# Kernel optimization log

Hardware: AMD Instinct MI355X
Metric: run time of the kernel (lower is better)

Reference implementation:

```python
import jax, jax.numpy as jnp
import numpy as np

B, L, C = 4, 2048, 1024
H = 16
D = C // H  # head_dim = 64


def _rope(t, cos, sin):
    # t: [B, H, L, D]; cos/sin: [L, D//2] broadcast to [1, 1, L, D//2]
    te = t[..., ::2]
    to = t[..., 1::2]
    c = cos[None, None]
    s = sin[None, None]
    re = te * c - to * s
    ro = te * s + to * c
    # interleave even/odd back: [..., D//2, 2] -> [..., D]
    return jnp.stack([re, ro], axis=-1).reshape(t.shape)


def setup_inputs() -> dict:
    key = jax.random.key(0)
    ks = jax.random.split(key, 5)
    x = jax.random.normal(ks[0], (B, L, C), dtype=jnp.float32)
    # rotary phases: theta_i = 10000^(-2i/D), angles = pos * theta
    inv_freq = 1.0 / (10000.0 ** (np.arange(0, D, 2, dtype=np.float32) / D))
    ang = np.arange(L, dtype=np.float32)[:, None] * inv_freq[None, :]  # [L, D//2]
    cos = jnp.asarray(np.cos(ang))
    sin = jnp.asarray(np.sin(ang))
    w_qkv = jax.random.normal(ks[1], (3 * C, C), dtype=jnp.float32) * (C ** -0.5)
    w_proj = jax.random.normal(ks[2], (C, C), dtype=jnp.float32) * (C ** -0.5)
    b_proj = jnp.zeros((C,), dtype=jnp.float32)
    return {"x": x, "cos": cos, "sin": sin, "w_qkv": w_qkv, "w_proj": w_proj, "b_proj": b_proj}


def reference(x, cos, sin, w_qkv, w_proj, b_proj):
    Bx, Lx, Cx = x.shape
    # QKV projection (torch Linear: y = x @ W.T), then split heads
    qkv = jnp.einsum("blc,fc->blf", x, w_qkv)  # [B, L, 3C]
    qkv = qkv.reshape(Bx, Lx, 3, H, D).transpose(2, 0, 3, 1, 4)  # [3, B, H, L, D]
    q, k, v = qkv[0], qkv[1], qkv[2]
    q = _rope(q, cos, sin)
    k = _rope(k, cos, sin)
    # scaled dot-product attention, non-causal
    scale = D ** -0.5
    scores = jnp.einsum("bhqd,bhkd->bhqk", q, k) * scale
    attn = jax.nn.softmax(scores, axis=-1)
    o = jnp.einsum("bhqk,bhkd->bhqd", attn, v)  # [B, H, L, D]
    o = o.transpose(0, 2, 1, 3).reshape(Bx, Lx, Cx)
    return jnp.einsum("blc,fc->blf", o, w_proj) + b_proj
```

## Files before the change

kernel.cpp:

```cpp
#include <hip/hip_runtime.h>
#include <hip/hip_bf16.h>
#include <cstdint>


typedef unsigned short u16;
typedef __attribute__((ext_vector_type(8))) short bf16x8;
typedef __attribute__((ext_vector_type(4))) float f32x4;
typedef __attribute__((ext_vector_type(2))) unsigned int u32x2;

#define GLD16(g, l)                                                            \
  __builtin_amdgcn_global_load_lds(                                            \
      (const __attribute__((address_space(1))) void*)(g),                      \
      (__attribute__((address_space(3))) void*)(l), 16, 0, 0)

static __device__ __forceinline__ u16 f32_bf16(float f) {
  union { float f; unsigned u; } v; v.f = f;
  unsigned r = v.u + 0x7FFFu + ((v.u >> 16) & 1u);
  return (u16)(r >> 16);
}
static __device__ __forceinline__ float bf16_f32(u16 h) {
  union { unsigned u; float f; } v; v.u = ((unsigned)h) << 16;
  return v.f;
}
static __device__ __forceinline__ unsigned pack_rne(float a, float b) {
  union { float f; unsigned u; } x, y; x.f = a; y.f = b;
  unsigned ua = x.u + 0x7FFFu + ((x.u >> 16) & 1u);
  unsigned ub = y.u + 0x7FFFu + ((y.u >> 16) & 1u);
  return (ua >> 16) | (ub & 0xFFFF0000u);
}
static __device__ __forceinline__ unsigned pack_bf16_hw(float a, float b) {
  float2 t; t.x = a; t.y = b;
  __hip_bfloat162 h = __float22bfloat162_rn(t);
  union { __hip_bfloat162 h; unsigned u; } c; c.h = h;
  return c.u;
}

__global__ __launch_bounds__(256) void convert_all(
    const void* __restrict__ x, const void* __restrict__ wq,
    const void* __restrict__ wp, const void* __restrict__ cs,
    const void* __restrict__ sn, const void* __restrict__ bs,
    u16* __restrict__ xb, u16* __restrict__ wqb, u16* __restrict__ wpb,
    u16* __restrict__ cb, u16* __restrict__ sb, u16* __restrict__ bb) {
  const unsigned f32mode = (((const unsigned*)cs)[0] == 0x3F800000u);
  int blk = blockIdx.x;
  if (blk >= 12288 && blk < 12416) {
    const void* src = (blk < 12352) ? cs : sn;
    u16* dst = (blk < 12352) ? cb : sb;
    int i = (blk - ((blk < 12352) ? 12288 : 12352)) * 256 + threadIdx.x;
    u16 e[4];
    if (f32mode) {
      float4 v = ((const float4*)src)[i];
      const float* vf = (const float*)&v;
#pragma unroll
      for (int c = 0; c < 4; c++) e[c] = f32_bf16(vf[c]);
    } else {
      uint2 v = ((const uint2*)src)[i];
      e[0] = (u16)(v.x & 0xFFFFu); e[1] = (u16)(v.x >> 16);
      e[2] = (u16)(v.y & 0xFFFFu); e[3] = (u16)(v.y >> 16);
    }
#pragma unroll
    for (int c = 0; c < 4; c++) {
      int E = i * 4 + c;
      dst[(E & 31) * 2048 + (E >> 5)] = e[c];
    }
    return;
  }
  const void* src; u16* dst; int i0, n4;
  if (blk < 8192)       { src = x;  dst = xb;  i0 = blk;         n4 = 2097152; }
  else if (blk < 11264) { src = wq; dst = wqb; i0 = blk - 8192;  n4 = 786432; }
  else if (blk < 12288) { src = wp; dst = wpb; i0 = blk - 11264; n4 = 262144; }
  else                  { src = bs; dst = bb;  i0 = blk - 12416; n4 = 256; }
  int i = i0 * 256 + threadIdx.x;
  if (i >= n4) return;
  if (f32mode) {
    float4 v = ((const float4*)src)[i];
    uint2 o;
    o.x = pack_rne(v.x, v.y);
    o.y = pack_rne(v.z, v.w);
    ((uint2*)dst)[i] = o;
  } else {
    ((uint2*)dst)[i] = ((const uint2*)src)[i];
  }
}

static __device__ __forceinline__ void gemm_mainloop(
    const u16* __restrict__ A, const u16* __restrict__ Bm, int K,
    int m0, int n0, u16* As, u16* Bs, f32x4 acc[4][4]) {
  const int tid  = threadIdx.x;
  const int lane = tid & 63;
  const int wave = tid >> 6;
  const int n16  = lane & 15;
  const int quad = lane >> 4;
  const int wm = (wave >> 1) * 64;
  const int wn = (wave & 1) * 64;
  const u16* ag = A  + (size_t)(m0 + wave * 16 + (lane >> 2)) * K + (lane & 3) * 8;
  const u16* bg = Bm + (size_t)(n0 + wave * 16 + (lane >> 2)) * K + (lane & 3) * 8;
  u16* al = As + wave * (16 * 32);
  u16* bl = Bs + wave * (16 * 32);
  for (int kt = 0; kt < K; kt += 32) {
    GLD16(ag + kt, al);
    GLD16(ag + (size_t)64 * K + kt, al + 64 * 32);
    GLD16(bg + kt, bl);
    GLD16(bg + (size_t)64 * K + kt, bl + 64 * 32);
    __syncthreads();
    bf16x8 af[4], bf[4];
#pragma unroll
    for (int i = 0; i < 4; i++)
      af[i] = *(const bf16x8*)(As + (wm + i * 16 + n16) * 32 + quad * 8);
#pragma unroll
    for (int j = 0; j < 4; j++)
      bf[j] = *(const bf16x8*)(Bs + (wn + j * 16 + n16) * 32 + quad * 8);
#pragma unroll
    for (int i = 0; i < 4; i++)
#pragma unroll
      for (int j = 0; j < 4; j++)
        acc[i][j] = __builtin_amdgcn_mfma_f32_16x16x32_bf16(af[i], bf[j], acc[i][j], 0, 0, 0);
    __syncthreads();
  }
}

__global__ __launch_bounds__(256) void gemm_qkv(
    const u16* __restrict__ x, const u16* __restrict__ w,
    u16* __restrict__ q_ws, u16* __restrict__ k_ws, u16* __restrict__ vt_ws,
    const u16* __restrict__ cosT, const u16* __restrict__ sinT) {
  __shared__ u16 As[128 * 32];
  __shared__ u16 Bs[128 * 32];
  f32x4 acc[4][4];
#pragma unroll
  for (int i = 0; i < 4; i++)
#pragma unroll
    for (int j = 0; j < 4; j++) acc[i][j] = (f32x4){0.f, 0.f, 0.f, 0.f};
  const int m0 = blockIdx.y * 128;
  const int n0 = blockIdx.x * 128;
  gemm_mainloop(x, w, 1024, m0, n0, As, Bs, acc);
  const int lane = threadIdx.x & 63, wave = threadIdx.x >> 6;
  const int n16 = lane & 15, quad = lane >> 4;
  const int wm = (wave >> 1) * 64, wn = (wave & 1) * 64;
#pragma unroll
  for (int i = 0; i < 4; i++)
#pragma unroll
    for (int j = 0; j < 4; j++) {
      int f = n0 + wn + j * 16 + n16;
      int which = f >> 10;
      int rem = f & 1023;
      int h = rem >> 6, d = rem & 63;
      int l0 = m0 + wm + i * 16 + quad * 4;
      int b = l0 >> 11, l = l0 & 2047;
      if (which == 2) {
        uint2 o;
        o.x = pack_rne(acc[i][j][0], acc[i][j][1]);
        o.y = pack_rne(acc[i][j][2], acc[i][j][3]);
        size_t idx = (((size_t)b * 16 + h) * 64 + d) * 2048 + l;
        *(uint2*)(vt_ws + idx) = o;
      } else {
        u16* dst = (which == 0) ? q_ws : k_ws;
        const float sc = (which == 0) ? 0.18033688011112042f : 1.0f;
        const int ip = d >> 1;
        const bool ev = !(d & 1);
        uint2 cu = *(const uint2*)(cosT + ip * 2048 + l);
        uint2 su = *(const uint2*)(sinT + ip * 2048 + l);
        float cf[4] = {bf16_f32((u16)(cu.x & 0xFFFFu)), bf16_f32((u16)(cu.x >> 16)),
                       bf16_f32((u16)(cu.y & 0xFFFFu)), bf16_f32((u16)(cu.y >> 16))};
        float sf[4] = {bf16_f32((u16)(su.x & 0xFFFFu)), bf16_f32((u16)(su.x >> 16)),
                       bf16_f32((u16)(su.y & 0xFFFFu)), bf16_f32((u16)(su.y >> 16))};
        size_t base = (((size_t)b * 16 + h) * 2048 + l) * 64 + d;
#pragma unroll
        for (int r = 0; r < 4; r++) {
          float v = acc[i][j][r];
          float p = __shfl_xor(v, 1, 64);
          float o = ev ? (v * cf[r] - p * sf[r]) : (p * sf[r] + v * cf[r]);
          dst[base + (size_t)r * 64] = f32_bf16(o * sc);
        }
      }
    }
}

__global__ __launch_bounds__(256, 4) void flash_attn(
    const u16* __restrict__ q_ws, const u16* __restrict__ k_ws,
    const u16* __restrict__ vt_ws, u16* __restrict__ o_ws) {
  __shared__ u16 Ks[2][64 * 64];
  __shared__ u16 Vs[2][64 * 64];
  const int bh = blockIdx.x & 63;
  const int q0 = (blockIdx.x >> 6) * 128;
  const int b = bh >> 4, h = bh & 15;
  const int tid = threadIdx.x, lane = tid & 63, wave = tid >> 6;
  const int n16 = lane & 15, quad = lane >> 4;
  const int x7 = n16 & 7;
  const int pn16 = (n16 & 3) | ((n16 & 4) << 1) | ((n16 & 8) >> 1);
  const int px7 = pn16 & 7;
  const size_t hoff = (size_t)bh * (2048 * 64);

  bf16x8 qf[2][2];
#pragma unroll
  for (int qb = 0; qb < 2; qb++) {
    const u16* qrow = q_ws + hoff + (size_t)(q0 + wave * 32 + qb * 16 + n16) * 64;
    qf[qb][0] = *(const bf16x8*)(qrow + quad * 8);
    qf[qb][1] = *(const bf16x8*)(qrow + 32 + quad * 8);
  }

  f32x4 oacc[2][4];
  f32x4 lq[2];
#pragma unroll
  for (int qb = 0; qb < 2; qb++) {
    lq[qb] = (f32x4){0.f, 0.f, 0.f, 0.f};
#pragma unroll
    for (int s = 0; s < 4; s++) oacc[qb][s] = (f32x4){0.f, 0.f, 0.f, 0.f};
  }

  const int srow = wave * 8 + (lane >> 3);
  const int sw = (lane & 7) ^ ((lane >> 3) & 7);
  const u16* kg = k_ws + hoff + (size_t)srow * 64 + sw * 8;
  const u16* vg = vt_ws + hoff + (size_t)srow * 2048 + sw * 8;
  const int loff = wave * 8 * 64;

  GLD16(kg, &Ks[0][loff]);
  GLD16(kg + 32 * 64, &Ks[0][loff + 32 * 64]);
  GLD16(vg, &Vs[0][loff]);
  GLD16(vg + (size_t)32 * 2048, &Vs[0][loff + 32 * 64]);

  for (int kt = 0; kt < 2048; kt += 64) {
    const int buf = (kt >> 6) & 1;
    __syncthreads();
    if (kt + 64 < 2048) {
      const u16* kgn = kg + (size_t)(kt + 64) * 64;
      const u16* vgn = vg + (kt + 64);
      GLD16(kgn, &Ks[buf ^ 1][loff]);
      GLD16(kgn + 32 * 64, &Ks[buf ^ 1][loff + 32 * 64]);
      GLD16(vgn, &Vs[buf ^ 1][loff]);
      GLD16(vgn + (size_t)32 * 2048, &Vs[buf ^ 1][loff + 32 * 64]);
    }
    const u16* ks = Ks[buf];
    const u16* vs = Vs[buf];

    unsigned pxk[2][4], pyk[2][4];
#pragma unroll
    for (int sub = 0; sub < 4; sub++) {
      const u16* krow = ks + (sub * 16 + pn16) * 64;
      bf16x8 kf0 = *(const bf16x8*)(krow + (quad ^ px7) * 8);
      bf16x8 kf1 = *(const bf16x8*)(krow + ((quad + 4) ^ px7) * 8);
#pragma unroll
      for (int qb = 0; qb < 2; qb++) {
        f32x4 z = (f32x4){0.f, 0.f, 0.f, 0.f};
        z = __builtin_amdgcn_mfma_f32_16x16x32_bf16(kf0, qf[qb][0], z, 0, 0, 0);
        z = __builtin_amdgcn_mfma_f32_16x16x32_bf16(kf1, qf[qb][1], z, 0, 0, 0);
        f32x4 p;
#pragma unroll
        for (int r = 0; r < 4; r++) p[r] = __builtin_amdgcn_exp2f(z[r]);
        lq[qb] += p;
        pxk[qb][sub] = pack_bf16_hw(p[0], p[1]);
        pyk[qb][sub] = pack_bf16_hw(p[2], p[3]);
      }
    }

    bf16x8 pf[2][2];
#pragma unroll
    for (int qb = 0; qb < 2; qb++) {
      u32x2 r0 = __builtin_amdgcn_permlane32_swap(pxk[qb][0], pxk[qb][1], false, false);
      u32x2 r1 = __builtin_amdgcn_permlane32_swap(pyk[qb][0], pyk[qb][1], false, false);
      u32x2 r2 = __builtin_amdgcn_permlane32_swap(pxk[qb][2], pxk[qb][3], false, false);
      u32x2 r3 = __builtin_amdgcn_permlane32_swap(pyk[qb][2], pyk[qb][3], false, false);
      union { unsigned u[4]; bf16x8 v; } t0, t1;
      t0.u[0] = r0.x; t0.u[1] = r1.x; t0.u[2] = r0.y; t0.u[3] = r1.y;
      t1.u[0] = r2.x; t1.u[1] = r3.x; t1.u[2] = r2.y; t1.u[3] = r3.y;
      pf[qb][0] = t0.v;
      pf[qb][1] = t1.v;
    }

#pragma unroll
    for (int sd = 0; sd < 4; sd++) {
      const u16* vrow = vs + (sd * 16 + n16) * 64;
      bf16x8 vf0 = *(const bf16x8*)(vrow + (quad ^ x7) * 8);
      bf16x8 vf1 = *(const bf16x8*)(vrow + ((quad + 4) ^ x7) * 8);
#pragma unroll
      for (int qb = 0; qb < 2; qb++) {
        oacc[qb][sd] = __builtin_amdgcn_mfma_f32_16x16x32_bf16(pf[qb][0], vf0, oacc[qb][sd], 0, 0, 0);
        oacc[qb][sd] = __builtin_amdgcn_mfma_f32_16x16x32_bf16(pf[qb][1], vf1, oacc[qb][sd], 0, 0, 0);
      }
    }
  }

#pragma unroll
  for (int qb = 0; qb < 2; qb++) {
    float l = lq[qb][0] + lq[qb][1] + lq[qb][2] + lq[qb][3];
    l += __shfl_xor(l, 16, 64);
    l += __shfl_xor(l, 32, 64);
    float linv = 1.0f / l;
#pragma unroll
    for (int r = 0; r < 4; r++) {
      float lr = __shfl(linv, quad * 4 + r, 64);
      int row = q0 + wave * 32 + qb * 16 + quad * 4 + r;
      size_t base = ((size_t)b * 2048 + row) * 1024 + h * 64;
#pragma unroll
      for (int sd = 0; sd < 4; sd++)
        o_ws[base + sd * 16 + n16] = f32_bf16(oacc[qb][sd][r] * lr);
    }
  }
}

__global__ __launch_bounds__(256) void gemm_proj(
    const u16* __restrict__ o, const u16* __restrict__ w,
    const u16* __restrict__ bias, float* __restrict__ out) {
  __shared__ u16 As[128 * 32];
  __shared__ u16 Bs[128 * 32];
  f32x4 acc[4][4];
#pragma unroll
  for (int i = 0; i < 4; i++)
#pragma unroll
    for (int j = 0; j < 4; j++) acc[i][j] = (f32x4){0.f, 0.f, 0.f, 0.f};
  const int m0 = blockIdx.y * 128;
  const int n0 = blockIdx.x * 128;
  gemm_mainloop(o, w, 1024, m0, n0, As, Bs, acc);
  const int lane = threadIdx.x & 63, wave = threadIdx.x >> 6;
  const int n16 = lane & 15, quad = lane >> 4;
  const int wm = (wave >> 1) * 64, wn = (wave & 1) * 64;
#pragma unroll
  for (int i = 0; i < 4; i++)
#pragma unroll
    for (int j = 0; j < 4; j++) {
      int f = n0 + wn + j * 16 + n16;
      float bf = bf16_f32(bias[f]);
#pragma unroll
      for (int r = 0; r < 4; r++) {
        int m = m0 + wm + i * 16 + quad * 4 + r;
        out[(size_t)m * 1024 + f] = acc[i][j][r] + bf;
      }
    }
}

extern "C" void kernel_launch(void* const* d_in, const int* in_sizes, int n_in,
                              void* d_out, int out_size, void* d_ws, size_t ws_size,
                              hipStream_t stream) {
  float* out = (float*)d_out;

  u16* ws = (u16*)d_ws;
  u16* xb     = ws;
  u16* wqkvb  = ws + 8388608;
  u16* wprojb = ws + 11534336;
  u16* cosb   = ws + 12582912;
  u16* sinb   = ws + 12648448;
  u16* biasb  = ws + 12713984;
  u16* qb     = ws + 12715008;
  u16* kb     = ws + 21103616;
  u16* vtb    = ws + 29492224;
  u16* ob     = xb;

  convert_all<<<12417, 256, 0, stream>>>(
      d_in[0], d_in[3], d_in[4], d_in[1], d_in[2], d_in[5],
      xb, wqkvb, wprojb, cosb, sinb, biasb);

  gemm_qkv<<<dim3(24, 64), 256, 0, stream>>>(xb, wqkvb, qb, kb, vtb, cosb, sinb);
  flash_attn<<<1024, 256, 0, stream>>>(qb, kb, vtb, ob);
  gemm_proj<<<dim3(8, 64), 256, 0, stream>>>(ob, wprojb, biasb, out);
}
```

Baseline: 293.3 us.

## Triple-buffer LDS in GEMM mainloop with async global-to-LDS prefetch

Converts the shared GEMM mainloop used by the QKV and output projections from a single LDS buffer to a three-stage ring. Tiles are prefetched two iterations ahead with global_load_lds, and a partial vmcnt wait plus one barrier per iteration replaces the two __syncthreads. The aim is to hide global load latency behind the MFMA work. In exchange, LDS use per block triples, which may lower occupancy, and the attention kernel is unchanged.

```diff
diff --git a/kernel.cpp b/kernel.cpp
--- a/kernel.cpp
+++ b/kernel.cpp
@@ -95,36 +95,57 @@
   const int wn = (wave & 1) * 64;
   const u16* ag = A  + (size_t)(m0 + wave * 16 + (lane >> 2)) * K + (lane & 3) * 8;
   const u16* bg = Bm + (size_t)(n0 + wave * 16 + (lane >> 2)) * K + (lane & 3) * 8;
-  u16* al = As + wave * (16 * 32);
-  u16* bl = Bs + wave * (16 * 32);
+  const int wl = wave * 512;
+
+#define STAGE_QKV(bufidx, ktoff)                                               \
+  {                                                                            \
+    u16* a_ = As + (bufidx) * 4096 + wl;                                       \
+    u16* b_ = Bs + (bufidx) * 4096 + wl;                                       \
+    GLD16(ag + (ktoff), a_);                                                   \
+    GLD16(ag + (size_t)64 * K + (ktoff), a_ + 64 * 32);                        \
+    GLD16(bg + (ktoff), b_);                                                   \
+    GLD16(bg + (size_t)64 * K + (ktoff), b_ + 64 * 32);                        \
+  }
+
+  STAGE_QKV(0, 0);
+  STAGE_QKV(1, 32);
+  int c0 = 0;
+  int c2 = 2;
   for (int kt = 0; kt < K; kt += 32) {
-    GLD16(ag + kt, al);
-    GLD16(ag + (size_t)64 * K + kt, al + 64 * 32);
-    GLD16(bg + kt, bl);
-    GLD16(bg + (size_t)64 * K + kt, bl + 64 * 32);
-    __syncthreads();
+    if (kt + 32 < K) {
+      asm volatile("s_waitcnt vmcnt(4)" ::: "memory");
+    } else {
+      asm volatile("s_waitcnt vmcnt(0)" ::: "memory");
+    }
+    __builtin_amdgcn_s_barrier();
+    __builtin_amdgcn_sched_barrier(0);
+    if (kt + 64 < K) STAGE_QKV(c2, kt + 64);
+    const u16* as = As + c0 * 4096;
+    const u16* bs = Bs + c0 * 4096;
     bf16x8 af[4], bf[4];
 #pragma unroll
     for (int i = 0; i < 4; i++)
-      af[i] = *(const bf16x8*)(As + (wm + i * 16 + n16) * 32 + quad * 8);
+      af[i] = *(const bf16x8*)(as + (wm + i * 16 + n16) * 32 + quad * 8);
 #pragma unroll
     for (int j = 0; j < 4; j++)
-      bf[j] = *(const bf16x8*)(Bs + (wn + j * 16 + n16) * 32 + quad * 8);
+      bf[j] = *(const bf16x8*)(bs + (wn + j * 16 + n16) * 32 + quad * 8);
 #pragma unroll
     for (int i = 0; i < 4; i++)
 #pragma unroll
       for (int j = 0; j < 4; j++)
         acc[i][j] = __builtin_amdgcn_mfma_f32_16x16x32_bf16(af[i], bf[j], acc[i][j], 0, 0, 0);
-    __syncthreads();
-  }
+    c0 = (c0 == 2) ? 0 : c0 + 1;
+    c2 = (c2 == 2) ? 0 : c2 + 1;
+  }
+#undef STAGE_QKV
 }
 
 __global__ __launch_bounds__(256) void gemm_qkv(
     const u16* __restrict__ x, const u16* __restrict__ w,
     u16* __restrict__ q_ws, u16* __restrict__ k_ws, u16* __restrict__ vt_ws,
     const u16* __restrict__ cosT, const u16* __restrict__ sinT) {
-  __shared__ u16 As[128 * 32];
-  __shared__ u16 Bs[128 * 32];
+  __shared__ u16 As[3 * 128 * 32];
+  __shared__ u16 Bs[3 * 128 * 32];
   f32x4 acc[4][4];
 #pragma unroll
   for (int i = 0; i < 4; i++)
@@ -300,8 +321,8 @@
 __global__ __launch_bounds__(256) void gemm_proj(
     const u16* __restrict__ o, const u16* __restrict__ w,
     const u16* __restrict__ bias, float* __restrict__ out) {
-  __shared__ u16 As[128 * 32];
-  __shared__ u16 Bs[128 * 32];
+  __shared__ u16 As[3 * 128 * 32];
+  __shared__ u16 Bs[3 * 128 * 32];
   f32x4 acc[4][4];
 #pragma unroll
   for (int i = 0; i < 4; i++)
```

Measured after the change: 293.2 us. Within noise of the previous version (-0.0%).
